# Optimization experiments

Measured on AMD Instinct MI355X. Metric: run time of the kernel, lower is better.

Reference implementation:

```python
import jax, jax.numpy as jnp
import numpy as np

N_NODES = 100000
N_EDGES = 1600000
H = 64
N_LAYERS = 3
NUM_APPS = max(1, N_LAYERS - 1)  # forward applies layer once, then while l>1 loop


def setup_inputs() -> dict:
    key = jax.random.key(0)
    k1, k2, k3, k4, k5 = jax.random.split(key, 5)
    features = jax.random.normal(k1, (N_NODES, H), dtype=jnp.float32)
    W = jax.random.normal(k2, (H, H), dtype=jnp.float32) / np.sqrt(H)
    b = jax.random.normal(k3, (H,), dtype=jnp.float32) * 0.01
    src = jax.random.randint(k4, (N_EDGES,), 0, N_NODES, dtype=jnp.int64)
    dst = jax.random.randint(k5, (N_EDGES,), 0, N_NODES, dtype=jnp.int64)
    return {"features": features, "W": W, "b": b, "src": src, "dst": dst}


def reference(features, W, b, src, dst):
    n = features.shape[0]
    ones = jnp.ones(src.shape[0], dtype=features.dtype)
    # DGL GraphConv norm='both': symmetric normalization, degrees clamped >= 1
    deg_out = jax.ops.segment_sum(ones, src, num_segments=n)
    deg_in = jax.ops.segment_sum(ones, dst, num_segments=n)
    inv_sqrt_out = jnp.clip(deg_out, 1.0, None) ** -0.5  # [N]
    inv_sqrt_in = jnp.clip(deg_in, 1.0, None) ** -0.5    # [N]

    h = features
    for _ in range(NUM_APPS):  # shared-weight GraphConv + ReLU, applied n_layers-1 times
        msg = (h * inv_sqrt_out[:, None])[src]                   # [E, H] gather
        agg = jax.ops.segment_sum(msg, dst, num_segments=n)      # [N, H] scatter-add
        h = jax.nn.relu((agg * inv_sqrt_in[:, None]) @ W + b)    # [N, H]
    return h
```

## Files before the change

kernel.cpp:

```cpp
#include <hip/hip_runtime.h>
#include <hip/hip_fp16.h>

#define N_NODES 100000
#define N_EDGES 1600000
#define HDIM 64
#define NPB 512
#define NPB_SHIFT 9
#define NBUCK 196
#define CAP 16384
#define NCHUNK 256
#define CHUNK (N_EDGES / NCHUNK)

__global__ void init_kernel(int* __restrict__ gcurD, int* __restrict__ gcurS) {
    int t = threadIdx.x;
    if (t < NBUCK) {
        gcurD[t] = t * CAP;
        gcurS[t] = t * CAP;
    }
}

__global__ void place_kernel(const int* __restrict__ src, const int* __restrict__ dst,
                             int* __restrict__ gcurD, int* __restrict__ gcurS,
                             unsigned int* __restrict__ bufD, unsigned short* __restrict__ bufS) {
    __shared__ int hD[NBUCK], hS[NBUCK], curD[NBUCK], curS[NBUCK];
    int t = threadIdx.x, blk = blockIdx.x;
    for (int i = t; i < NBUCK; i += 256) { hD[i] = 0; hS[i] = 0; }
    __syncthreads();
    int e0 = blk * CHUNK;
    for (int i = t; i < CHUNK; i += 256) {
        atomicAdd(&hD[dst[e0 + i] >> NPB_SHIFT], 1);
        atomicAdd(&hS[src[e0 + i] >> NPB_SHIFT], 1);
    }
    __syncthreads();
    for (int i = t; i < NBUCK; i += 256) {
        curD[i] = hD[i] ? atomicAdd(&gcurD[i], hD[i]) : 0;
        curS[i] = hS[i] ? atomicAdd(&gcurS[i], hS[i]) : 0;
    }
    __syncthreads();
    for (int i = t; i < CHUNK; i += 256) {
        int s = src[e0 + i], d = dst[e0 + i];
        int pd = atomicAdd(&curD[d >> NPB_SHIFT], 1);
        bufD[pd] = (unsigned)s | ((unsigned)(d & (NPB - 1)) << 17);
        int ps = atomicAdd(&curS[s >> NPB_SHIFT], 1);
        bufS[ps] = (unsigned short)(s & (NPB - 1));
    }
}

__global__ void bucket_kernel(const unsigned int* __restrict__ bufD,
                              const unsigned short* __restrict__ bufS,
                              const int* __restrict__ gcurD, const int* __restrict__ gcurS,
                              int* __restrict__ csr_src, int2* __restrict__ offs,
                              float* __restrict__ inv_in, float* __restrict__ inv_out) {
    __shared__ int cnt[NPB], pre[NPB], cur[NPB];
    int t = threadIdx.x;
    int blk = blockIdx.x;
    if (blk < NBUCK) {
        int b = blk;
        int ebase = b * CAP;
        int ecnt  = gcurD[b] - ebase;
        cnt[t] = 0;
        __syncthreads();
        for (int i = t; i < ecnt; i += NPB)
            atomicAdd(&cnt[(int)(bufD[ebase + i] >> 17)], 1);
        __syncthreads();
        int v = cnt[t];
        pre[t] = v;
        __syncthreads();
        for (int off = 1; off < NPB; off <<= 1) {
            int x = (t >= off) ? pre[t - off] : 0;
            __syncthreads(); pre[t] += x; __syncthreads();
        }
        int excl = pre[t] - v;
        cur[t] = excl;
        int node = b * NPB + t;
        if (node < N_NODES) {
            offs[node] = make_int2(ebase + excl, ebase + excl + v);
            inv_in[node] = rsqrtf((float)max(v, 1));
        }
        __syncthreads();
        for (int i = t; i < ecnt; i += NPB) {
            unsigned en = bufD[ebase + i];
            int pos = atomicAdd(&cur[(int)(en >> 17)], 1);
            csr_src[ebase + pos] = (int)(en & 0x1FFFFu);
        }
    } else {
        int b = blk - NBUCK;
        int ebase = b * CAP;
        int ecnt  = gcurS[b] - ebase;
        cnt[t] = 0;
        __syncthreads();
        for (int i = t; i < ecnt; i += NPB)
            atomicAdd(&cnt[(int)bufS[ebase + i]], 1);
        __syncthreads();
        int node = b * NPB + t;
        if (node < N_NODES) inv_out[node] = rsqrtf((float)max(cnt[t], 1));
    }
}

__device__ inline uint2 f4_to_h4(float4 a) {
    __half2 lo = __floats2half2_rn(a.x, a.y);
    __half2 hi = __floats2half2_rn(a.z, a.w);
    uint2 r;
    r.x = *(unsigned*)&lo;
    r.y = *(unsigned*)&hi;
    return r;
}

__global__ void dense_kernel(const float* __restrict__ h, const float* __restrict__ inv_out,
                             const float* __restrict__ W, uint2* __restrict__ hw, int n) {
    __shared__ float Wlds[HDIM * HDIM];
    __shared__ float Alds[32][HDIM + 1];
    int t = threadIdx.x;
    int r0 = blockIdx.x * 32;

    for (int i = t; i < HDIM * HDIM / 4; i += 256)
        ((float4*)Wlds)[i] = ((const float4*)W)[i];

    for (int i = t; i < 512; i += 256) {
        int r = i >> 4;
        int c4 = i & 15;
        int row = r0 + r;
        float4 v = make_float4(0.f, 0.f, 0.f, 0.f);
        float s = 0.f;
        if (row < n) {
            v = ((const float4*)h)[(long long)row * 16 + c4];
            s = inv_out[row];
        }
        Alds[r][c4 * 4 + 0] = v.x * s;
        Alds[r][c4 * 4 + 1] = v.y * s;
        Alds[r][c4 * 4 + 2] = v.z * s;
        Alds[r][c4 * 4 + 3] = v.w * s;
    }
    __syncthreads();

    int tx = t & 15;
    int ty = t >> 4;
    float4 acc0 = make_float4(0.f, 0.f, 0.f, 0.f);
    float4 acc1 = acc0;

#pragma unroll 8
    for (int k = 0; k < HDIM; ++k) {
        float4 w = ((const float4*)(Wlds + k * HDIM))[tx];
        float a0 = Alds[2 * ty + 0][k];
        float a1 = Alds[2 * ty + 1][k];
        acc0.x = fmaf(a0, w.x, acc0.x); acc0.y = fmaf(a0, w.y, acc0.y);
        acc0.z = fmaf(a0, w.z, acc0.z); acc0.w = fmaf(a0, w.w, acc0.w);
        acc1.x = fmaf(a1, w.x, acc1.x); acc1.y = fmaf(a1, w.y, acc1.y);
        acc1.z = fmaf(a1, w.z, acc1.z); acc1.w = fmaf(a1, w.w, acc1.w);
    }

    int rb = r0 + 2 * ty;
    if (rb + 0 < n) hw[(long long)(rb + 0) * 16 + tx] = f4_to_h4(acc0);
    if (rb + 1 < n) hw[(long long)(rb + 1) * 16 + tx] = f4_to_h4(acc1);
}

__global__ void gather_kernel(const uint4* __restrict__ hw, const float* __restrict__ inv_in,
                              const int2* __restrict__ offs, const int* __restrict__ csr_src,
                              const float* __restrict__ bias, float* __restrict__ out, int n) {
    int t = threadIdx.x;
    int wave = t >> 6, lane = t & 63;
    int g = lane >> 3, gl = lane & 7;
    int row = blockIdx.x * 32 + wave * 8 + g;
    if (row >= n) return;

    float acc0 = 0.f, acc1 = 0.f, acc2 = 0.f, acc3 = 0.f;
    float acc4 = 0.f, acc5 = 0.f, acc6 = 0.f, acc7 = 0.f;

    int2 oe = offs[row];
    int start = oe.x, end = oe.y;
    int gbase = g << 3;

    int jb = start;
    int mm = end - jb; if (mm > 8) mm = 8;
    int sidx = (mm > 0 && gl < mm) ? csr_src[jb + gl] : 0;

    while (jb < end) {
        int jb2 = jb + 8;
        int mm2 = end - jb2; if (mm2 > 8) mm2 = 8;
        int sidx2 = (jb2 < end && gl < mm2) ? csr_src[jb2 + gl] : 0;

        if (mm == 8) {
#pragma unroll
            for (int j = 0; j < 8; ++j) {
                int s = __shfl(sidx, gbase + j, 64);
                uint4 u = hw[(long long)s * 8 + gl];
                float2 f0 = __half22float2(*(__half2*)&u.x);
                float2 f1 = __half22float2(*(__half2*)&u.y);
                float2 f2 = __half22float2(*(__half2*)&u.z);
                float2 f3 = __half22float2(*(__half2*)&u.w);
                acc0 += f0.x; acc1 += f0.y; acc2 += f1.x; acc3 += f1.y;
                acc4 += f2.x; acc5 += f2.y; acc6 += f3.x; acc7 += f3.y;
            }
        } else {
            for (int j = 0; j < mm; ++j) {
                int s = __shfl(sidx, gbase + j, 64);
                uint4 u = hw[(long long)s * 8 + gl];
                float2 f0 = __half22float2(*(__half2*)&u.x);
                float2 f1 = __half22float2(*(__half2*)&u.y);
                float2 f2 = __half22float2(*(__half2*)&u.z);
                float2 f3 = __half22float2(*(__half2*)&u.w);
                acc0 += f0.x; acc1 += f0.y; acc2 += f1.x; acc3 += f1.y;
                acc4 += f2.x; acc5 += f2.y; acc6 += f3.x; acc7 += f3.y;
            }
        }
        jb = jb2; mm = mm2; sidx = sidx2;
    }

    float sc = inv_in[row];
    float4 b0 = ((const float4*)bias)[gl * 2 + 0];
    float4 b1 = ((const float4*)bias)[gl * 2 + 1];
    float4 r0, r1;
    r0.x = fmaxf(fmaf(acc0, sc, b0.x), 0.f);
    r0.y = fmaxf(fmaf(acc1, sc, b0.y), 0.f);
    r0.z = fmaxf(fmaf(acc2, sc, b0.z), 0.f);
    r0.w = fmaxf(fmaf(acc3, sc, b0.w), 0.f);
    r1.x = fmaxf(fmaf(acc4, sc, b1.x), 0.f);
    r1.y = fmaxf(fmaf(acc5, sc, b1.y), 0.f);
    r1.z = fmaxf(fmaf(acc6, sc, b1.z), 0.f);
    r1.w = fmaxf(fmaf(acc7, sc, b1.w), 0.f);
    ((float4*)out)[(long long)row * 16 + gl * 2 + 0] = r0;
    ((float4*)out)[(long long)row * 16 + gl * 2 + 1] = r1;
}

extern "C" void kernel_launch(void* const* d_in, const int* in_sizes, int n_in,
                              void* d_out, int out_size, void* d_ws, size_t ws_size,
                              hipStream_t stream) {
    const float* features = (const float*)d_in[0];
    const float* W        = (const float*)d_in[1];
    const float* b        = (const float*)d_in[2];
    const int*   src      = (const int*)d_in[3];
    const int*   dst      = (const int*)d_in[4];

    float* out = (float*)d_out;

    float* ws = (float*)d_ws;
    uint2* hw = (uint2*)ws;
    unsigned int*   bufD = (unsigned int*)(ws + (size_t)N_NODES * 32);
    unsigned short* bufS = (unsigned short*)(bufD + (size_t)NBUCK * CAP);
    int*   csr_src = (int*)(bufS + (size_t)NBUCK * CAP);
    int2*  offs    = (int2*)(csr_src + (size_t)NBUCK * CAP);
    float* inv_out = (float*)(offs + N_NODES);
    float* inv_in  = inv_out + N_NODES;
    int*   gcurD   = (int*)(inv_in + N_NODES);
    int*   gcurS   = gcurD + NBUCK;

    const int N = N_NODES;

    init_kernel<<<1, 256, 0, stream>>>(gcurD, gcurS);
    place_kernel<<<NCHUNK, 256, 0, stream>>>(src, dst, gcurD, gcurS, bufD, bufS);
    bucket_kernel<<<2 * NBUCK, NPB, 0, stream>>>(bufD, bufS, gcurD, gcurS,
                                                 csr_src, offs, inv_in, inv_out);

    int dense_blocks  = (N + 31) / 32;
    int gather_blocks = (N + 31) / 32;

    dense_kernel<<<dense_blocks, 256, 0, stream>>>(features, inv_out, W, hw, N);
    gather_kernel<<<gather_blocks, 256, 0, stream>>>((const uint4*)hw, inv_in, offs, csr_src, b, out, N);

    dense_kernel<<<dense_blocks, 256, 0, stream>>>(out, inv_out, W, hw, N);
    gather_kernel<<<gather_blocks, 256, 0, stream>>>((const uint4*)hw, inv_in, offs, csr_src, b, out, N);
}
```

Baseline: 235.2 us.

## Fuse first dense GEMM into edge placement kernel; apply source norm in gather

Result: no change. 239.6 us (+1.9%).

```diff
diff --git a/kernel.cpp b/kernel.cpp
--- a/kernel.cpp
+++ b/kernel.cpp
@@ -11,6 +11,8 @@
 #define NCHUNK 256
 #define CHUNK (N_EDGES / NCHUNK)
 
+typedef float f4v __attribute__((ext_vector_type(4)));
+
 __global__ void init_kernel(int* __restrict__ gcurD, int* __restrict__ gcurS) {
     int t = threadIdx.x;
     if (t < NBUCK) {
@@ -19,31 +21,96 @@
     }
 }
 
-__global__ void place_kernel(const int* __restrict__ src, const int* __restrict__ dst,
-                             int* __restrict__ gcurD, int* __restrict__ gcurS,
-                             unsigned int* __restrict__ bufD, unsigned short* __restrict__ bufS) {
-    __shared__ int hD[NBUCK], hS[NBUCK], curD[NBUCK], curS[NBUCK];
+__device__ inline uint2 f4_to_h4(float x, float y, float z, float w) {
+    __half2 lo = __floats2half2_rn(x, y);
+    __half2 hi = __floats2half2_rn(z, w);
+    uint2 r;
+    r.x = *(unsigned*)&lo;
+    r.y = *(unsigned*)&hi;
+    return r;
+}
+
+__device__ __forceinline__ void dense_body(int t, int r0,
+                                           const float* __restrict__ h,
+                                           const float* __restrict__ W,
+                                           uint2* __restrict__ hw, int n) {
+    __shared__ float Wlds[HDIM * HDIM];
+    __shared__ float Alds[32][HDIM + 1];
+
+    for (int i = t; i < HDIM * HDIM / 4; i += 256)
+        ((f4v*)Wlds)[i] = ((const f4v*)W)[i];
+
+    for (int i = t; i < 512; i += 256) {
+        int r = i >> 4;
+        int c4 = i & 15;
+        int row = r0 + r;
+        f4v v = {0.f, 0.f, 0.f, 0.f};
+        if (row < n)
+            v = __builtin_nontemporal_load((const f4v*)h + (long long)row * 16 + c4);
+        Alds[r][c4 * 4 + 0] = v.x;
+        Alds[r][c4 * 4 + 1] = v.y;
+        Alds[r][c4 * 4 + 2] = v.z;
+        Alds[r][c4 * 4 + 3] = v.w;
+    }
+    __syncthreads();
+
+    int tx = t & 15;
+    int ty = t >> 4;
+    float4 acc0 = make_float4(0.f, 0.f, 0.f, 0.f);
+    float4 acc1 = acc0;
+
+#pragma unroll 8
+    for (int k = 0; k < HDIM; ++k) {
+        f4v w = ((const f4v*)(Wlds + k * HDIM))[tx];
+        float a0 = Alds[2 * ty + 0][k];
+        float a1 = Alds[2 * ty + 1][k];
+        acc0.x = fmaf(a0, w.x, acc0.x); acc0.y = fmaf(a0, w.y, acc0.y);
+        acc0.z = fmaf(a0, w.z, acc0.z); acc0.w = fmaf(a0, w.w, acc0.w);
+        acc1.x = fmaf(a1, w.x, acc1.x); acc1.y = fmaf(a1, w.y, acc1.y);
+        acc1.z = fmaf(a1, w.z, acc1.z); acc1.w = fmaf(a1, w.w, acc1.w);
+    }
+
+    int rb = r0 + 2 * ty;
+    if (rb + 0 < n) hw[(long long)(rb + 0) * 16 + tx] = f4_to_h4(acc0.x, acc0.y, acc0.z, acc0.w);
+    if (rb + 1 < n) hw[(long long)(rb + 1) * 16 + tx] = f4_to_h4(acc1.x, acc1.y, acc1.z, acc1.w);
+}
+
+__global__ void place_dense_kernel(const int* __restrict__ src, const int* __restrict__ dst,
+                                   int* __restrict__ gcurD, int* __restrict__ gcurS,
+                                   unsigned int* __restrict__ bufD, unsigned short* __restrict__ bufS,
+                                   const float* __restrict__ h, const float* __restrict__ W,
+                                   uint2* __restrict__ hw, int n) {
     int t = threadIdx.x, blk = blockIdx.x;
-    for (int i = t; i < NBUCK; i += 256) { hD[i] = 0; hS[i] = 0; }
-    __syncthreads();
-    int e0 = blk * CHUNK;
-    for (int i = t; i < CHUNK; i += 256) {
-        atomicAdd(&hD[dst[e0 + i] >> NPB_SHIFT], 1);
-        atomicAdd(&hS[src[e0 + i] >> NPB_SHIFT], 1);
-    }
-    __syncthreads();
-    for (int i = t; i < NBUCK; i += 256) {
-        curD[i] = hD[i] ? atomicAdd(&gcurD[i], hD[i]) : 0;
-        curS[i] = hS[i] ? atomicAdd(&gcurS[i], hS[i]) : 0;
-    }
-    __syncthreads();
-    for (int i = t; i < CHUNK; i += 256) {
-        int s = src[e0 + i], d = dst[e0 + i];
-        int pd = atomicAdd(&curD[d >> NPB_SHIFT], 1);
-        bufD[pd] = (unsigned)s | ((unsigned)(d & (NPB - 1)) << 17);
-        int ps = atomicAdd(&curS[s >> NPB_SHIFT], 1);
-        bufS[ps] = (unsigned short)(s & (NPB - 1));
-    }
+    if (blk < NCHUNK) {
+        __shared__ int hD[NBUCK], hS[NBUCK], curD[NBUCK], curS[NBUCK];
+        for (int i = t; i < NBUCK; i += 256) { hD[i] = 0; hS[i] = 0; }
+        __syncthreads();
+        int e0 = blk * CHUNK;
+        for (int i = t; i < CHUNK; i += 256) {
+            atomicAdd(&hD[dst[e0 + i] >> NPB_SHIFT], 1);
+            atomicAdd(&hS[src[e0 + i] >> NPB_SHIFT], 1);
+        }
+        __syncthreads();
+        for (int i = t; i < NBUCK; i += 256) {
+            curD[i] = hD[i] ? atomicAdd(&gcurD[i], hD[i]) : 0;
+            curS[i] = hS[i] ? atomicAdd(&gcurS[i], hS[i]) : 0;
+        }
+        __syncthreads();
+        for (int i = t; i < CHUNK; i += 256) {
+            int s = src[e0 + i], d = dst[e0 + i];
+            int pd = atomicAdd(&curD[d >> NPB_SHIFT], 1);
+            bufD[pd] = (unsigned)s | ((unsigned)(d & (NPB - 1)) << 17);
+            int ps = atomicAdd(&curS[s >> NPB_SHIFT], 1);
+            bufS[ps] = (unsigned short)(s & (NPB - 1));
+        }
+    } else {
+        dense_body(t, (blk - NCHUNK) * 32, h, W, hw, n);
+    }
+}
+
+__global__ void dense_kernel(const float* __restrict__ h, const float* __restrict__ W,
+                             uint2* __restrict__ hw, int n) {
+    dense_body(threadIdx.x, blockIdx.x * 32, h, W, hw, n);
 }
 
 __global__ void bucket_kernel(const unsigned int* __restrict__ bufD,
@@ -97,64 +164,8 @@
     }
 }
 
-__device__ inline uint2 f4_to_h4(float4 a) {
-    __half2 lo = __floats2half2_rn(a.x, a.y);
-    __half2 hi = __floats2half2_rn(a.z, a.w);
-    uint2 r;
-    r.x = *(unsigned*)&lo;
-    r.y = *(unsigned*)&hi;
-    return r;
-}
-
-__global__ void dense_kernel(const float* __restrict__ h, const float* __restrict__ inv_out,
-                             const float* __restrict__ W, uint2* __restrict__ hw, int n) {
-    __shared__ float Wlds[HDIM * HDIM];
-    __shared__ float Alds[32][HDIM + 1];
-    int t = threadIdx.x;
-    int r0 = blockIdx.x * 32;
-
-    for (int i = t; i < HDIM * HDIM / 4; i += 256)
-        ((float4*)Wlds)[i] = ((const float4*)W)[i];
-
-    for (int i = t; i < 512; i += 256) {
-        int r = i >> 4;
-        int c4 = i & 15;
-        int row = r0 + r;
-        float4 v = make_float4(0.f, 0.f, 0.f, 0.f);
-        float s = 0.f;
-        if (row < n) {
-            v = ((const float4*)h)[(long long)row * 16 + c4];
-            s = inv_out[row];
-        }
-        Alds[r][c4 * 4 + 0] = v.x * s;
-        Alds[r][c4 * 4 + 1] = v.y * s;
-        Alds[r][c4 * 4 + 2] = v.z * s;
-        Alds[r][c4 * 4 + 3] = v.w * s;
-    }
-    __syncthreads();
-
-    int tx = t & 15;
-    int ty = t >> 4;
-    float4 acc0 = make_float4(0.f, 0.f, 0.f, 0.f);
-    float4 acc1 = acc0;
-
-#pragma unroll 8
-    for (int k = 0; k < HDIM; ++k) {
-        float4 w = ((const float4*)(Wlds + k * HDIM))[tx];
-        float a0 = Alds[2 * ty + 0][k];
-        float a1 = Alds[2 * ty + 1][k];
-        acc0.x = fmaf(a0, w.x, acc0.x); acc0.y = fmaf(a0, w.y, acc0.y);
-        acc0.z = fmaf(a0, w.z, acc0.z); acc0.w = fmaf(a0, w.w, acc0.w);
-        acc1.x = fmaf(a1, w.x, acc1.x); acc1.y = fmaf(a1, w.y, acc1.y);
-        acc1.z = fmaf(a1, w.z, acc1.z); acc1.w = fmaf(a1, w.w, acc1.w);
-    }
-
-    int rb = r0 + 2 * ty;
-    if (rb + 0 < n) hw[(long long)(rb + 0) * 16 + tx] = f4_to_h4(acc0);
-    if (rb + 1 < n) hw[(long long)(rb + 1) * 16 + tx] = f4_to_h4(acc1);
-}
-
 __global__ void gather_kernel(const uint4* __restrict__ hw, const float* __restrict__ inv_in,
+                              const float* __restrict__ inv_out,
                               const int2* __restrict__ offs, const int* __restrict__ csr_src,
                               const float* __restrict__ bias, float* __restrict__ out, int n) {
     int t = threadIdx.x;
@@ -173,43 +184,51 @@
     int jb = start;
     int mm = end - jb; if (mm > 8) mm = 8;
     int sidx = (mm > 0 && gl < mm) ? csr_src[jb + gl] : 0;
+    float sw = inv_out[sidx];
 
     while (jb < end) {
         int jb2 = jb + 8;
         int mm2 = end - jb2; if (mm2 > 8) mm2 = 8;
         int sidx2 = (jb2 < end && gl < mm2) ? csr_src[jb2 + gl] : 0;
+        float sw2 = inv_out[sidx2];
 
         if (mm == 8) {
 #pragma unroll
             for (int j = 0; j < 8; ++j) {
                 int s = __shfl(sidx, gbase + j, 64);
+                float w = __shfl(sw, gbase + j, 64);
                 uint4 u = hw[(long long)s * 8 + gl];
                 float2 f0 = __half22float2(*(__half2*)&u.x);
                 float2 f1 = __half22float2(*(__half2*)&u.y);
                 float2 f2 = __half22float2(*(__half2*)&u.z);
                 float2 f3 = __half22float2(*(__half2*)&u.w);
-                acc0 += f0.x; acc1 += f0.y; acc2 += f1.x; acc3 += f1.y;
-                acc4 += f2.x; acc5 += f2.y; acc6 += f3.x; acc7 += f3.y;
+                acc0 = fmaf(f0.x, w, acc0); acc1 = fmaf(f0.y, w, acc1);
+                acc2 = fmaf(f1.x, w, acc2); acc3 = fmaf(f1.y, w, acc3);
+                acc4 = fmaf(f2.x, w, acc4); acc5 = fmaf(f2.y, w, acc5);
+                acc6 = fmaf(f3.x, w, acc6); acc7 = fmaf(f3.y, w, acc7);
             }
         } else {
             for (int j = 0; j < mm; ++j) {
                 int s = __shfl(sidx, gbase + j, 64);
+                float w = __shfl(sw, gbase + j, 64);
                 uint4 u = hw[(long long)s * 8 + gl];
                 float2 f0 = __half22float2(*(__half2*)&u.x);
                 float2 f1 = __half22float2(*(__half2*)&u.y);
                 float2 f2 = __half22float2(*(__half2*)&u.z);
                 float2 f3 = __half22float2(*(__half2*)&u.w);
-                acc0 += f0.x; acc1 += f0.y; acc2 += f1.x; acc3 += f1.y;
-                acc4 += f2.x; acc5 += f2.y; acc6 += f3.x; acc7 += f3.y;
+                acc0 = fmaf(f0.x, w, acc0); acc1 = fmaf(f0.y, w, acc1);
+                acc2 = fmaf(f1.x, w, acc2); acc3 = fmaf(f1.y, w, acc3);
+                acc4 = fmaf(f2.x, w, acc4); acc5 = fmaf(f2.y, w, acc5);
+                acc6 = fmaf(f3.x, w, acc6); acc7 = fmaf(f3.y, w, acc7);
             }
         }
-        jb = jb2; mm = mm2; sidx = sidx2;
+        jb = jb2; mm = mm2; sidx = sidx2; sw = sw2;
     }
 
     float sc = inv_in[row];
     float4 b0 = ((const float4*)bias)[gl * 2 + 0];
     float4 b1 = ((const float4*)bias)[gl * 2 + 1];
-    float4 r0, r1;
+    f4v r0, r1;
     r0.x = fmaxf(fmaf(acc0, sc, b0.x), 0.f);
     r0.y = fmaxf(fmaf(acc1, sc, b0.y), 0.f);
     r0.z = fmaxf(fmaf(acc2, sc, b0.z), 0.f);
@@ -218,8 +237,8 @@
     r1.y = fmaxf(fmaf(acc5, sc, b1.y), 0.f);
     r1.z = fmaxf(fmaf(acc6, sc, b1.z), 0.f);
     r1.w = fmaxf(fmaf(acc7, sc, b1.w), 0.f);
-    ((float4*)out)[(long long)row * 16 + gl * 2 + 0] = r0;
-    ((float4*)out)[(long long)row * 16 + gl * 2 + 1] = r1;
+    __builtin_nontemporal_store(r0, (f4v*)out + (long long)row * 16 + gl * 2 + 0);
+    __builtin_nontemporal_store(r1, (f4v*)out + (long long)row * 16 + gl * 2 + 1);
 }
 
 extern "C" void kernel_launch(void* const* d_in, const int* in_sizes, int n_in,
@@ -245,18 +264,21 @@
     int*   gcurS   = gcurD + NBUCK;
 
     const int N = N_NODES;
+    int dense_blocks  = (N + 31) / 32;
+    int gather_blocks = (N + 31) / 32;
 
     init_kernel<<<1, 256, 0, stream>>>(gcurD, gcurS);
-    place_kernel<<<NCHUNK, 256, 0, stream>>>(src, dst, gcurD, gcurS, bufD, bufS);
+
+    place_dense_kernel<<<NCHUNK + dense_blocks, 256, 0, stream>>>(
+        src, dst, gcurD, gcurS, bufD, bufS, features, W, hw, N);
+
     bucket_kernel<<<2 * NBUCK, NPB, 0, stream>>>(bufD, bufS, gcurD, gcurS,
                                                  csr_src, offs, inv_in, inv_out);
 
-    int dense_blocks  = (N + 31) / 32;
-    int gather_blocks = (N + 31) / 32;
-
-    dense_kernel<<<dense_blocks, 256, 0, stream>>>(features, inv_out, W, hw, N);
-    gather_kernel<<<gather_blocks, 256, 0, stream>>>((const uint4*)hw, inv_in, offs, csr_src, b, out, N);
-
-    dense_kernel<<<dense_blocks, 256, 0, stream>>>(out, inv_out, W, hw, N);
-    gather_kernel<<<gather_blocks, 256, 0, stream>>>((const uint4*)hw, inv_in, offs, csr_src, b, out, N);
-}
+    gather_kernel<<<gather_blocks, 256, 0, stream>>>((const uint4*)hw, inv_in, inv_out,
+                                                     offs, csr_src, b, out, N);
+
+    dense_kernel<<<dense_blocks, 256, 0, stream>>>(out, W, hw, N);
+    gather_kernel<<<gather_blocks, 256, 0, stream>>>((const uint4*)hw, inv_in, inv_out,
+                                                     offs, csr_src, b, out, N);
+}
```

## Fuse first-layer gather with second-layer dense transform into one kernel

Applied to the files above, without the earlier changes.

Measured after the change: 229.9 us. -2.2%, faster.

```diff
diff --git a/kernel.cpp b/kernel.cpp
--- a/kernel.cpp
+++ b/kernel.cpp
@@ -11,12 +11,23 @@
 #define NCHUNK 256
 #define CHUNK (N_EDGES / NCHUNK)
 
+typedef float f4v __attribute__((ext_vector_type(4)));
+
 __global__ void init_kernel(int* __restrict__ gcurD, int* __restrict__ gcurS) {
     int t = threadIdx.x;
     if (t < NBUCK) {
         gcurD[t] = t * CAP;
         gcurS[t] = t * CAP;
     }
+}
+
+__device__ inline uint2 f4_to_h4(float x, float y, float z, float w) {
+    __half2 lo = __floats2half2_rn(x, y);
+    __half2 hi = __floats2half2_rn(z, w);
+    uint2 r;
+    r.x = *(unsigned*)&lo;
+    r.y = *(unsigned*)&hi;
+    return r;
 }
 
 __global__ void place_kernel(const int* __restrict__ src, const int* __restrict__ dst,
@@ -97,15 +108,6 @@
     }
 }
 
-__device__ inline uint2 f4_to_h4(float4 a) {
-    __half2 lo = __floats2half2_rn(a.x, a.y);
-    __half2 hi = __floats2half2_rn(a.z, a.w);
-    uint2 r;
-    r.x = *(unsigned*)&lo;
-    r.y = *(unsigned*)&hi;
-    return r;
-}
-
 __global__ void dense_kernel(const float* __restrict__ h, const float* __restrict__ inv_out,
                              const float* __restrict__ W, uint2* __restrict__ hw, int n) {
     __shared__ float Wlds[HDIM * HDIM];
@@ -114,16 +116,16 @@
     int r0 = blockIdx.x * 32;
 
     for (int i = t; i < HDIM * HDIM / 4; i += 256)
-        ((float4*)Wlds)[i] = ((const float4*)W)[i];
+        ((f4v*)Wlds)[i] = ((const f4v*)W)[i];
 
     for (int i = t; i < 512; i += 256) {
         int r = i >> 4;
         int c4 = i & 15;
         int row = r0 + r;
-        float4 v = make_float4(0.f, 0.f, 0.f, 0.f);
+        f4v v = {0.f, 0.f, 0.f, 0.f};
         float s = 0.f;
         if (row < n) {
-            v = ((const float4*)h)[(long long)row * 16 + c4];
+            v = __builtin_nontemporal_load((const f4v*)h + (long long)row * 16 + c4);
             s = inv_out[row];
         }
         Alds[r][c4 * 4 + 0] = v.x * s;
@@ -140,7 +142,7 @@
 
 #pragma unroll 8
     for (int k = 0; k < HDIM; ++k) {
-        float4 w = ((const float4*)(Wlds + k * HDIM))[tx];
+        f4v w = ((const f4v*)(Wlds + k * HDIM))[tx];
         float a0 = Alds[2 * ty + 0][k];
         float a1 = Alds[2 * ty + 1][k];
         acc0.x = fmaf(a0, w.x, acc0.x); acc0.y = fmaf(a0, w.y, acc0.y);
@@ -150,8 +152,99 @@
     }
 
     int rb = r0 + 2 * ty;
-    if (rb + 0 < n) hw[(long long)(rb + 0) * 16 + tx] = f4_to_h4(acc0);
-    if (rb + 1 < n) hw[(long long)(rb + 1) * 16 + tx] = f4_to_h4(acc1);
+    if (rb + 0 < n) hw[(long long)(rb + 0) * 16 + tx] = f4_to_h4(acc0.x, acc0.y, acc0.z, acc0.w);
+    if (rb + 1 < n) hw[(long long)(rb + 1) * 16 + tx] = f4_to_h4(acc1.x, acc1.y, acc1.z, acc1.w);
+}
+
+__global__ void gather_dense_kernel(const uint4* __restrict__ hw_in, const float* __restrict__ inv_in,
+                                    const float* __restrict__ inv_out,
+                                    const int2* __restrict__ offs, const int* __restrict__ csr_src,
+                                    const float* __restrict__ bias, const float* __restrict__ W,
+                                    uint2* __restrict__ hw_out, int n) {
+    __shared__ float Wlds[HDIM * HDIM];
+    int t = threadIdx.x;
+    for (int i = t; i < HDIM * HDIM / 4; i += 256)
+        ((f4v*)Wlds)[i] = ((const f4v*)W)[i];
+
+    int wave = t >> 6, lane = t & 63;
+    int g = lane >> 3, gl = lane & 7;
+    int row = blockIdx.x * 32 + wave * 8 + g;
+
+    float acc0 = 0.f, acc1 = 0.f, acc2 = 0.f, acc3 = 0.f;
+    float acc4 = 0.f, acc5 = 0.f, acc6 = 0.f, acc7 = 0.f;
+
+    int2 oe = offs[row];
+    int start = oe.x, end = oe.y;
+    int gbase = g << 3;
+
+    int jb = start;
+    int mm = end - jb; if (mm > 8) mm = 8;
+    int sidx = (mm > 0 && gl < mm) ? csr_src[jb + gl] : 0;
+
+    while (jb < end) {
+        int jb2 = jb + 8;
+        int mm2 = end - jb2; if (mm2 > 8) mm2 = 8;
+        int sidx2 = (jb2 < end && gl < mm2) ? csr_src[jb2 + gl] : 0;
+
+        if (mm == 8) {
+#pragma unroll
+            for (int j = 0; j < 8; ++j) {
+                int s = __shfl(sidx, gbase + j, 64);
+                uint4 u = hw_in[(long long)s * 8 + gl];
+                float2 f0 = __half22float2(*(__half2*)&u.x);
+                float2 f1 = __half22float2(*(__half2*)&u.y);
+                float2 f2 = __half22float2(*(__half2*)&u.z);
+                float2 f3 = __half22float2(*(__half2*)&u.w);
+                acc0 += f0.x; acc1 += f0.y; acc2 += f1.x; acc3 += f1.y;
+                acc4 += f2.x; acc5 += f2.y; acc6 += f3.x; acc7 += f3.y;
+            }
+        } else {
+            for (int j = 0; j < mm; ++j) {
+                int s = __shfl(sidx, gbase + j, 64);
+                uint4 u = hw_in[(long long)s * 8 + gl];
+                float2 f0 = __half22float2(*(__half2*)&u.x);
+                float2 f1 = __half22float2(*(__half2*)&u.y);
+                float2 f2 = __half22float2(*(__half2*)&u.z);
+                float2 f3 = __half22float2(*(__half2*)&u.w);
+                acc0 += f0.x; acc1 += f0.y; acc2 += f1.x; acc3 += f1.y;
+                acc4 += f2.x; acc5 += f2.y; acc6 += f3.x; acc7 += f3.y;
+            }
+        }
+        jb = jb2; mm = mm2; sidx = sidx2;
+    }
+
+    float sc = inv_in[row];
+    float so = inv_out[row];
+    float4 b0 = ((const float4*)bias)[gl * 2 + 0];
+    float4 b1 = ((const float4*)bias)[gl * 2 + 1];
+    f4v h0, h1;
+    h0.x = fmaxf(fmaf(acc0, sc, b0.x), 0.f) * so;
+    h0.y = fmaxf(fmaf(acc1, sc, b0.y), 0.f) * so;
+    h0.z = fmaxf(fmaf(acc2, sc, b0.z), 0.f) * so;
+    h0.w = fmaxf(fmaf(acc3, sc, b0.w), 0.f) * so;
+    h1.x = fmaxf(fmaf(acc4, sc, b1.x), 0.f) * so;
+    h1.y = fmaxf(fmaf(acc5, sc, b1.y), 0.f) * so;
+    h1.z = fmaxf(fmaf(acc6, sc, b1.z), 0.f) * so;
+    h1.w = fmaxf(fmaf(acc7, sc, b1.w), 0.f) * so;
+
+    __syncthreads();
+
+    float d0 = 0.f, d1 = 0.f, d2 = 0.f, d3 = 0.f;
+    float d4 = 0.f, d5 = 0.f, d6 = 0.f, d7 = 0.f;
+#pragma unroll
+    for (int k = 0; k < HDIM; ++k) {
+        float av = ((k >> 2) & 1) ? h1[k & 3] : h0[k & 3];
+        float ak = __shfl(av, gbase + (k >> 3), 64);
+        f4v w0 = ((const f4v*)Wlds)[k * 16 + gl * 2 + 0];
+        f4v w1 = ((const f4v*)Wlds)[k * 16 + gl * 2 + 1];
+        d0 = fmaf(ak, w0.x, d0); d1 = fmaf(ak, w0.y, d1);
+        d2 = fmaf(ak, w0.z, d2); d3 = fmaf(ak, w0.w, d3);
+        d4 = fmaf(ak, w1.x, d4); d5 = fmaf(ak, w1.y, d5);
+        d6 = fmaf(ak, w1.z, d6); d7 = fmaf(ak, w1.w, d7);
+    }
+
+    hw_out[(long long)row * 16 + gl * 2 + 0] = f4_to_h4(d0, d1, d2, d3);
+    hw_out[(long long)row * 16 + gl * 2 + 1] = f4_to_h4(d4, d5, d6, d7);
 }
 
 __global__ void gather_kernel(const uint4* __restrict__ hw, const float* __restrict__ inv_in,
@@ -209,7 +302,7 @@
     float sc = inv_in[row];
     float4 b0 = ((const float4*)bias)[gl * 2 + 0];
     float4 b1 = ((const float4*)bias)[gl * 2 + 1];
-    float4 r0, r1;
+    f4v r0, r1;
     r0.x = fmaxf(fmaf(acc0, sc, b0.x), 0.f);
     r0.y = fmaxf(fmaf(acc1, sc, b0.y), 0.f);
     r0.z = fmaxf(fmaf(acc2, sc, b0.z), 0.f);
@@ -218,8 +311,8 @@
     r1.y = fmaxf(fmaf(acc5, sc, b1.y), 0.f);
     r1.z = fmaxf(fmaf(acc6, sc, b1.z), 0.f);
     r1.w = fmaxf(fmaf(acc7, sc, b1.w), 0.f);
-    ((float4*)out)[(long long)row * 16 + gl * 2 + 0] = r0;
-    ((float4*)out)[(long long)row * 16 + gl * 2 + 1] = r1;
+    __builtin_nontemporal_store(r0, (f4v*)out + (long long)row * 16 + gl * 2 + 0);
+    __builtin_nontemporal_store(r1, (f4v*)out + (long long)row * 16 + gl * 2 + 1);
 }
 
 extern "C" void kernel_launch(void* const* d_in, const int* in_sizes, int n_in,
@@ -234,8 +327,9 @@
     float* out = (float*)d_out;
 
     float* ws = (float*)d_ws;
-    uint2* hw = (uint2*)ws;
-    unsigned int*   bufD = (unsigned int*)(ws + (size_t)N_NODES * 32);
+    uint2* hw  = (uint2*)ws;
+    uint2* hw2 = (uint2*)(ws + (size_t)N_NODES * 32);
+    unsigned int*   bufD = (unsigned int*)(ws + (size_t)N_NODES * 64);
     unsigned short* bufS = (unsigned short*)(bufD + (size_t)NBUCK * CAP);
     int*   csr_src = (int*)(bufS + (size_t)NBUCK * CAP);
     int2*  offs    = (int2*)(csr_src + (size_t)NBUCK * CAP);
@@ -245,18 +339,21 @@
     int*   gcurS   = gcurD + NBUCK;
 
     const int N = N_NODES;
+    int dense_blocks  = (N + 31) / 32;
+    int gather_blocks = (N + 31) / 32;
 
     init_kernel<<<1, 256, 0, stream>>>(gcurD, gcurS);
+
     place_kernel<<<NCHUNK, 256, 0, stream>>>(src, dst, gcurD, gcurS, bufD, bufS);
+
     bucket_kernel<<<2 * NBUCK, NPB, 0, stream>>>(bufD, bufS, gcurD, gcurS,
                                                  csr_src, offs, inv_in, inv_out);
 
-    int dense_blocks  = (N + 31) / 32;
-    int gather_blocks = (N + 31) / 32;
-
     dense_kernel<<<dense_blocks, 256, 0, stream>>>(features, inv_out, W, hw, N);
-    gather_kernel<<<gather_blocks, 256, 0, stream>>>((const uint4*)hw, inv_in, offs, csr_src, b, out, N);
-
-    dense_kernel<<<dense_blocks, 256, 0, stream>>>(out, inv_out, W, hw, N);
-    gather_kernel<<<gather_blocks, 256, 0, stream>>>((const uint4*)hw, inv_in, offs, csr_src, b, out, N);
-}
+
+    gather_dense_kernel<<<gather_blocks, 256, 0, stream>>>(
+        (const uint4*)hw, inv_in, inv_out, offs, csr_src, b, W, hw2, N);
+
+    gather_kernel<<<gather_blocks, 256, 0, stream>>>(
+        (const uint4*)hw2, inv_in, offs, csr_src, b, out, N);
+}
```
